# Performance work log

Measured on AMD Instinct MI355X. Metric: run time of the kernel, lower is better.

Reference implementation:

```python
import jax, jax.numpy as jnp
import numpy as np
import math
from itertools import combinations

SEQ_LEN = 8
SET_SIZE = 3
IN_DIM = 2048
OUT_DIM = 1152
WAY = 5
SHOT = 5
N_QUERIES = 200
PE_SCALE = 0.1
LN_EPS = 1e-5
NEG_INF = -1e30

TUPLES = np.array(list(combinations(range(SEQ_LEN), SET_SIZE)), dtype=np.int32)  # [56, 3]
TUPLES_LEN = TUPLES.shape[0]


def _positional_encoding(d_model, max_len):
    position = np.arange(max_len)[:, None].astype(np.float32)
    div_term = np.exp(np.arange(0, d_model, 2).astype(np.float32) * -(math.log(10000.0) / d_model))
    pe = np.zeros((max_len, d_model), dtype=np.float32)
    pe[:, 0::2] = np.sin(position * div_term) * PE_SCALE
    pe[:, 1::2] = np.cos(position * div_term) * PE_SCALE
    return jnp.asarray(pe)

PE = _positional_encoding(IN_DIM, int(SEQ_LEN * 1.5))


def setup_inputs() -> dict:
    key = jax.random.key(0)
    ks = jax.random.split(key, 6)
    support_set = jax.random.normal(ks[0], (WAY * SHOT, SEQ_LEN, IN_DIM), dtype=jnp.float32)
    queries = jax.random.normal(ks[1], (N_QUERIES, SEQ_LEN, IN_DIM), dtype=jnp.float32)
    support_labels = jnp.repeat(jnp.arange(WAY, dtype=jnp.int32), SHOT)  # [25]
    Wk = jax.random.normal(ks[2], (IN_DIM * SET_SIZE, OUT_DIM), dtype=jnp.float32) * 0.02
    bk = jnp.zeros((OUT_DIM,), dtype=jnp.float32)
    Wv = jax.random.normal(ks[3], (IN_DIM * SET_SIZE, OUT_DIM), dtype=jnp.float32) * 0.02
    bv = jnp.zeros((OUT_DIM,), dtype=jnp.float32)
    ln_g = jnp.ones((OUT_DIM,), dtype=jnp.float32)
    ln_b = jnp.zeros((OUT_DIM,), dtype=jnp.float32)
    return {"support_set": support_set, "support_labels": support_labels, "queries": queries,
            "Wk": Wk, "bk": bk, "Wv": Wv, "bv": bv, "ln_g": ln_g, "ln_b": ln_b}


def _layernorm(x, g, b):
    mu = jnp.mean(x, axis=-1, keepdims=True)
    var = jnp.var(x, axis=-1, keepdims=True)
    return (x - mu) * jax.lax.rsqrt(var + LN_EPS) * g + b


def _tuple_features(x):
    # x: [N, SEQ_LEN, IN_DIM]; add PE (dropout is identity at inference), gather frame tuples.
    n = x.shape[0]
    x = x + PE[None, :x.shape[1], :]
    return x[:, TUPLES, :].reshape(n, TUPLES_LEN, SET_SIZE * IN_DIM)  # [N, 56, 6144]


def reference(support_set, support_labels, queries, Wk, bk, Wv, bv, ln_g, ln_b):
    n_q = queries.shape[0]
    s_feat = _tuple_features(support_set)   # [S, T, 6144]
    q_feat = _tuple_features(queries)       # [Q, T, 6144]

    sk = _layernorm(s_feat @ Wk + bk, ln_g, ln_b)  # [S, T, D]
    qk = _layernorm(q_feat @ Wk + bk, ln_g, ln_b)  # [Q, T, D]
    sv = s_feat @ Wv + bv                           # [S, T, D]
    qv = q_feat @ Wv + bv                           # [Q, T, D]

    # scores between every query tuple and every support tuple
    scores = jnp.einsum('qtd,skd->qtsk', qk, sk) / math.sqrt(OUT_DIM)  # [Q, T, S, T]

    # per-class masked softmax over (support clips of class c) x (support tuples)
    class_mask = support_labels[None, :] == jnp.arange(WAY, dtype=support_labels.dtype)[:, None]  # [WAY, S]
    masked = scores[None] + jnp.where(class_mask[:, None, None, :, None], 0.0, NEG_INF)  # [WAY, Q, T, S, T]
    attn = jax.nn.softmax(masked.reshape(WAY, n_q, TUPLES_LEN, -1), axis=-1)
    attn = attn.reshape(WAY, n_q, TUPLES_LEN, -1, TUPLES_LEN)  # [WAY, Q, T, S, T]

    proto = jnp.einsum('cqtsk,skd->cqtd', attn, sv)  # [WAY, Q, T, D]
    diff = qv[None] - proto                           # [WAY, Q, T, D]
    dist = -jnp.sum(diff * diff, axis=(2, 3)) / TUPLES_LEN  # [WAY, Q]
    return dist.T  # logits [Q, WAY]
```

## Files before the change

### kernel.cpp

```cpp
#include <hip/hip_runtime.h>
#include <math.h>

#define SEQ_LEN 8
#define IN_DIM 2048
#define OUT_DIM 1152
#define NTUP 56
#define NSUP 25
#define NQ 200
#define WAY 5
#define SFRAMES 200
#define NFRAMES 1800
#define SROWS 1400
#define QROWS 11200
#define AT_STRIDE 1440
#define KC 288
#define ALD 296

typedef __attribute__((ext_vector_type(8))) short short8;
typedef __attribute__((ext_vector_type(4))) float f32x4;

__device__ __constant__ int TUP[NTUP][3] = {
{0,1,2},{0,1,3},{0,1,4},{0,1,5},{0,1,6},{0,1,7},
{0,2,3},{0,2,4},{0,2,5},{0,2,6},{0,2,7},
{0,3,4},{0,3,5},{0,3,6},{0,3,7},
{0,4,5},{0,4,6},{0,4,7},
{0,5,6},{0,5,7},
{0,6,7},
{1,2,3},{1,2,4},{1,2,5},{1,2,6},{1,2,7},
{1,3,4},{1,3,5},{1,3,6},{1,3,7},
{1,4,5},{1,4,6},{1,4,7},
{1,5,6},{1,5,7},
{1,6,7},
{2,3,4},{2,3,5},{2,3,6},{2,3,7},
{2,4,5},{2,4,6},{2,4,7},
{2,5,6},{2,5,7},
{2,6,7},
{3,4,5},{3,4,6},{3,4,7},
{3,5,6},{3,5,7},
{3,6,7},
{4,5,6},{4,5,7},
{4,6,7},
{5,6,7}};

__device__ __forceinline__ unsigned short f2bf(float x) {
  union { float f; unsigned int u; } v; v.f = x;
  unsigned int r = v.u + 0x7fffu + ((v.u >> 16) & 1u);
  return (unsigned short)(r >> 16);
}
__device__ __forceinline__ float bf2f(unsigned short s) {
  union { float f; unsigned int u; } v; v.u = ((unsigned int)s) << 16;
  return v.f;
}

__device__ __forceinline__ void gll16(const void* g, void* l) {
  __builtin_amdgcn_global_load_lds(
      (const __attribute__((address_space(1))) unsigned int*)g,
      (__attribute__((address_space(3))) unsigned int*)l, 16, 0, 0);
}

#define VMCNT(N) asm volatile("s_waitcnt vmcnt(" #N ")" ::: "memory")

__device__ __forceinline__ void pbar() {
  asm volatile("" ::: "memory");
  __builtin_amdgcn_s_barrier();
  asm volatile("" ::: "memory");
}

#define APB_OFF   0UL
#define WT_OFF    7372800UL
#define PB_OFF    35684352UL
#define QKB_OFF   60567552UL
#define SKB_OFF   86372352UL
#define QVB_OFF   89597952UL
#define SVB_OFF   115402752UL
#define G2_OFF    118628352UL
#define SCB_OFF   119457792UL
#define G1B_OFF   151713792UL
#define QNORM_OFF 183969792UL
#define RANK_OFF  184014592UL

__global__ __launch_bounds__(256) void k_pre(const float* __restrict__ S,
                                             const float* __restrict__ Q,
                                             const float* __restrict__ Wk,
                                             const float* __restrict__ Wv,
                                             const int* __restrict__ labels,
                                             unsigned short* __restrict__ APb,
                                             unsigned short* __restrict__ WT,
                                             int* __restrict__ rank,
                                             float* __restrict__ outz) {
  __shared__ float t[32][33];
  int b = blockIdx.x, tid = threadIdx.x;
  if (b < NFRAMES) {
    int frame = b;
    int e8 = tid * 8;
    int pos = frame & 7;
    const float c0 = -logf(10000.0f) / (float)IN_DIM;
    float pe[8];
#pragma unroll
    for (int p = 0; p < 4; ++p) {
      float dt = expf((float)(e8 + 2 * p) * c0);
      float arg = (float)pos * dt;
      pe[2 * p] = sinf(arg) * 0.1f;
      pe[2 * p + 1] = cosf(arg) * 0.1f;
    }
    const float* src = (frame < SFRAMES) ? (S + (size_t)frame * IN_DIM + e8)
                                         : (Q + (size_t)(frame - SFRAMES) * IN_DIM + e8);
    float4 x0 = ((const float4*)src)[0], x1 = ((const float4*)src)[1];
    short8 o;
    o[0] = (short)f2bf(x0.x + pe[0]); o[1] = (short)f2bf(x0.y + pe[1]);
    o[2] = (short)f2bf(x0.z + pe[2]); o[3] = (short)f2bf(x0.w + pe[3]);
    o[4] = (short)f2bf(x1.x + pe[4]); o[5] = (short)f2bf(x1.y + pe[5]);
    o[6] = (short)f2bf(x1.z + pe[6]); o[7] = (short)f2bf(x1.w + pe[7]);
    *(short8*)(APb + (size_t)frame * IN_DIM + e8) = o;
  } else if (b < NFRAMES + 13824) {
    int z = b - NFRAMES;
    int bz = z / (64 * 36); int rem = z % (64 * 36);
    int by = rem / 64, bx = rem % 64;
    int w = bz / 3, j = bz % 3;
    const float* W = w ? Wv : Wk;
    int k0 = bx * 32, d0 = by * 32;
    int tx = tid & 31, ty = tid >> 5;
#pragma unroll
    for (int i = 0; i < 4; ++i) {
      int k = k0 + ty + i * 8;
      t[ty + i * 8][tx] = W[(size_t)(j * IN_DIM + k) * OUT_DIM + d0 + tx];
    }
    __syncthreads();
    int colbase = w * 3456 + j * 1152 + d0;
#pragma unroll
    for (int i = 0; i < 4; ++i) {
      int d = ty + i * 8;
      WT[(size_t)(colbase + d) * IN_DIM + k0 + tx] = f2bf(t[tx][d]);
    }
  } else {
    for (int i = tid; i < NQ * WAY; i += 256) outz[i] = 0.f;
    if (tid == 0) {
      for (int s = 0; s < NSUP; ++s) {
        int r = 0;
        for (int s2 = 0; s2 < NSUP; ++s2)
          r += (labels[s2] < labels[s]) || (labels[s2] == labels[s] && s2 < s);
        rank[s] = r;
      }
    }
  }
}

__device__ __forceinline__ void mfma_core(const short* __restrict__ A, int lda, int maxA,
                                          const short* __restrict__ B, int ldb, int maxB,
                                          int K, short* lds, f32x4 (&acc)[4][4]) {
  int tid = threadIdx.x;
  int lane = tid & 63, wave = tid >> 6;
  int wm = wave & 1, wn = wave >> 1;
  int col = lane & 15, quad = lane >> 4;
  int s0 = tid, s1 = tid + 256;
  int r0 = s0 >> 2, r1 = s1 >> 2;
  int o0 = (s0 & 3) * 8, o1 = (s1 & 3) * 8;
  const short* a0p = A + (size_t)min(r0, maxA) * lda + o0;
  const short* a1p = A + (size_t)min(r1, maxA) * lda + o1;
  const short* b0p = B + (size_t)min(r0, maxB) * ldb + o0;
  const short* b1p = B + (size_t)min(r1, maxB) * ldb + o1;
  const int nt = K >> 5;

#define STAGE(t)                                     \
  do {                                               \
    short* buf_ = lds + (((t) & 3) << 13);           \
    int k0_ = (t) << 5;                              \
    gll16(a0p + k0_, buf_ + s0 * 8);                 \
    gll16(a1p + k0_, buf_ + s1 * 8);                 \
    gll16(b0p + k0_, buf_ + 4096 + s0 * 8);          \
    gll16(b1p + k0_, buf_ + 4096 + s1 * 8);          \
  } while (0)

  STAGE(0);
  STAGE(1);
  VMCNT(4);
  pbar();

  for (int t = 0; t < nt; ++t) {
    if (t + 2 < nt) STAGE(t + 2);
    const short* As = lds + ((t & 3) << 13);
    const short* Bs = As + 4096;
    short8 af[4], bf[4];
#pragma unroll
    for (int i = 0; i < 4; ++i)
      af[i] = *(const short8*)(As + (wm * 64 + i * 16 + col) * 32 + quad * 8);
#pragma unroll
    for (int j = 0; j < 4; ++j)
      bf[j] = *(const short8*)(Bs + (wn * 64 + j * 16 + col) * 32 + quad * 8);
    __builtin_amdgcn_s_setprio(1);
#pragma unroll
    for (int i = 0; i < 4; ++i)
#pragma unroll
      for (int j = 0; j < 4; ++j)
        acc[i][j] = __builtin_amdgcn_mfma_f32_16x16x32_bf16(af[i], bf[j], acc[i][j], 0, 0, 0);
    __builtin_amdgcn_s_setprio(0);
    if (t + 2 < nt) VMCNT(4);
    else            VMCNT(0);
    pbar();
  }
#undef STAGE
}

__global__ __launch_bounds__(256) void k_gemm1(const unsigned short* __restrict__ APb,
                                               const unsigned short* __restrict__ WT,
                                               unsigned short* __restrict__ Pb) {
  __shared__ short lds[32768];
  int row0 = blockIdx.y * 128, col0 = blockIdx.x * 128;
  f32x4 acc[4][4];
#pragma unroll
  for (int i = 0; i < 4; ++i)
#pragma unroll
    for (int j = 0; j < 4; ++j) acc[i][j] = (f32x4)(0.f);
  mfma_core((const short*)APb + (size_t)row0 * IN_DIM, IN_DIM, min(127, NFRAMES - 1 - row0),
            (const short*)WT + (size_t)col0 * IN_DIM, IN_DIM, 127,
            IN_DIM, lds, acc);
  int lane = threadIdx.x & 63, wave = threadIdx.x >> 6;
  int wm = wave & 1, wn = wave >> 1, col = lane & 15, quad = lane >> 4;
#pragma unroll
  for (int i = 0; i < 4; ++i)
#pragma unroll
    for (int r = 0; r < 4; ++r) {
      int gr = row0 + wm * 64 + i * 16 + quad * 4 + r;
      if (gr >= NFRAMES) continue;
#pragma unroll
      for (int j = 0; j < 4; ++j)
        Pb[(size_t)gr * 6912 + col0 + wn * 64 + j * 16 + col] = f2bf(acc[i][j][r]);
    }
}

__global__ __launch_bounds__(256) void k_combine(const unsigned short* __restrict__ Pb,
                                                 const float* __restrict__ bk,
                                                 const float* __restrict__ bv,
                                                 const float* __restrict__ g,
                                                 const float* __restrict__ bb,
                                                 const int* __restrict__ rank,
                                                 unsigned short* __restrict__ SKb,
                                                 unsigned short* __restrict__ QKb,
                                                 unsigned short* __restrict__ SVb,
                                                 unsigned short* __restrict__ QVb,
                                                 float* __restrict__ qnorm) {
  __shared__ short L[8 * 3456];
  int n = blockIdx.x, w = blockIdx.y;
  int tid = threadIdx.x;
  bool sup = n < NSUP;
  int fbase = sup ? n * SEQ_LEN : SFRAMES + (n - NSUP) * SEQ_LEN;
  for (int i = 0; i < 14; ++i) {
    int idx = tid + 256 * i;
    if (idx < 3456) {
      int fr = idx / 432, off = (idx - fr * 432) * 8;
      *(short8*)(L + fr * 3456 + off) =
          *(const short8*)(Pb + (size_t)(fbase + fr) * 6912 + w * 3456 + off);
    }
  }
  __syncthreads();
  int wave = tid >> 6, lane = tid & 63;
  const float* bias = w ? bv : bk;
  float2 bi[9], gg[9], bbv[9];
#pragma unroll
  for (int i = 0; i < 9; ++i) {
    int p = lane + 64 * i;
    bi[i] = *(const float2*)(bias + 2 * p);
    if (w == 0) {
      gg[i] = *(const float2*)(g + 2 * p);
      bbv[i] = *(const float2*)(bb + 2 * p);
    }
  }
  int obase = sup ? rank[n] * NTUP : (n - NSUP) * NTUP;
  const unsigned int* Lu = (const unsigned int*)L;
  for (int t = wave; t < NTUP; t += 4) {
    int b0 = (TUP[t][0] * 3456) >> 1;
    int b1 = (TUP[t][1] * 3456 + 1152) >> 1;
    int b2 = (TUP[t][2] * 3456 + 2304) >> 1;
    float va[18];
    float sum = 0.f, sq = 0.f;
#pragma unroll
    for (int i = 0; i < 9; ++i) {
      int p = lane + 64 * i;
      unsigned int u0 = Lu[b0 + p], u1 = Lu[b1 + p], u2 = Lu[b2 + p];
      float a = bf2f((unsigned short)u0) + bf2f((unsigned short)u1) +
                bf2f((unsigned short)u2) + bi[i].x;
      float b = bf2f((unsigned short)(u0 >> 16)) + bf2f((unsigned short)(u1 >> 16)) +
                bf2f((unsigned short)(u2 >> 16)) + bi[i].y;
      va[2 * i] = a; va[2 * i + 1] = b;
      sum += a + b;
      sq += a * a + b * b;
    }
#pragma unroll
    for (int o = 32; o; o >>= 1) {
      sum += __shfl_xor(sum, o);
      sq += __shfl_xor(sq, o);
    }
    int orow = obase + t;
    if (w == 0) {
      float mean = sum * (1.f / OUT_DIM);
      float var = sq * (1.f / OUT_DIM) - mean * mean;
      float inv = rsqrtf(var + 1e-5f);
      unsigned short* outp = (sup ? SKb : QKb) + (size_t)orow * OUT_DIM;
#pragma unroll
      for (int i = 0; i < 9; ++i) {
        int p = lane + 64 * i;
        unsigned int lo = f2bf((va[2 * i] - mean) * inv * gg[i].x + bbv[i].x);
        unsigned int hi = f2bf((va[2 * i + 1] - mean) * inv * gg[i].y + bbv[i].y);
        *(unsigned int*)(outp + 2 * p) = lo | (hi << 16);
      }
    } else {
      unsigned short* outp = (sup ? SVb : QVb) + (size_t)orow * OUT_DIM;
#pragma unroll
      for (int i = 0; i < 9; ++i) {
        int p = lane + 64 * i;
        unsigned int lo = f2bf(va[2 * i]);
        unsigned int hi = f2bf(va[2 * i + 1]);
        *(unsigned int*)(outp + 2 * p) = lo | (hi << 16);
      }
      if (!sup && lane == 0) qnorm[orow] = sq;
    }
  }
}

__global__ __launch_bounds__(256) void k_rowgemm(const unsigned short* __restrict__ QKb,
                                                 const unsigned short* __restrict__ SKb,
                                                 const unsigned short* __restrict__ QVb,
                                                 const unsigned short* __restrict__ SVb,
                                                 unsigned short* __restrict__ SCb,
                                                 unsigned short* __restrict__ G1b,
                                                 unsigned short* __restrict__ G2) {
  __shared__ short lds[32768];
  int L = blockIdx.x;
  f32x4 acc[4][4];
#pragma unroll
  for (int i = 0; i < 4; ++i)
#pragma unroll
    for (int j = 0; j < 4; ++j) acc[i][j] = (f32x4)(0.f);
  int lane = threadIdx.x & 63, wave = threadIdx.x >> 6;
  int wm = wave & 1, wn = wave >> 1, col = lane & 15, quad = lane >> 4;

  if (L < 1936) {
    int l = L, g1 = 0;
    if (l >= 968) { g1 = 1; l -= 968; }
    int rowSub = l & 7, t = l >> 3;
    int colIdx = t % 11, rowGroup = t / 11;
    int row0 = (rowGroup * 8 + rowSub) << 7;
    int col0 = colIdx << 7;
    const unsigned short* Am = g1 ? QVb : QKb;
    const unsigned short* Bm = g1 ? SVb : SKb;
    mfma_core((const short*)Am + (size_t)row0 * OUT_DIM, OUT_DIM, min(127, QROWS - 1 - row0),
              (const short*)Bm + (size_t)col0 * OUT_DIM, OUT_DIM, min(127, SROWS - 1 - col0),
              OUT_DIM, lds, acc);
    unsigned short* outp = g1 ? G1b : SCb;
    const float scl = g1 ? 1.0f : 0.029462782549439483f;
#pragma unroll
    for (int i = 0; i < 4; ++i)
#pragma unroll
      for (int r = 0; r < 4; ++r) {
        int gr = row0 + wm * 64 + i * 16 + quad * 4 + r;
        if (gr >= QROWS) continue;
#pragma unroll
        for (int j = 0; j < 4; ++j) {
          int gc = col0 + wn * 64 + j * 16 + col;
          if (gc < SROWS) {
            int c = gc / 280;
            outp[(size_t)gr * AT_STRIDE + gc + c * 8] = f2bf(acc[i][j][r] * scl);
          }
        }
      }
  } else {
    int l = L - 1936;
    int c = l / 9, rem = l % 9;
    int i0 = (rem / 3) << 7, j0 = (rem % 3) << 7;
    const short* base = (const short*)SVb + (size_t)c * 280 * OUT_DIM;
    mfma_core(base + (size_t)i0 * OUT_DIM, OUT_DIM, min(127, 279 - i0),
              base + (size_t)j0 * OUT_DIM, OUT_DIM, min(127, 279 - j0),
              OUT_DIM, lds, acc);
    unsigned short* g2c = G2 + (size_t)c * KC * KC;
#pragma unroll
    for (int i = 0; i < 4; ++i)
#pragma unroll
      for (int r = 0; r < 4; ++r) {
        int gi = i0 + wm * 64 + i * 16 + quad * 4 + r;
        if (gi >= KC) continue;
#pragma unroll
        for (int j = 0; j < 4; ++j) {
          int gj = j0 + wn * 64 + j * 16 + col;
          if (gj < KC) g2c[(size_t)gi * KC + gj] = f2bf(acc[i][j][r]);
        }
      }
  }
}

__global__ __launch_bounds__(256) void k_attn(const unsigned short* __restrict__ SCb,
                                              const unsigned short* __restrict__ G1b,
                                              const unsigned short* __restrict__ G2,
                                              const float* __restrict__ qnorm,
                                              float* __restrict__ out) {
  __shared__ short attn[64 * ALD];
  __shared__ short Bs[64 * KC];
  __shared__ float T2n[64];
  __shared__ float Sarr[64];
  __shared__ float rowsum[64];
  __shared__ float val[64];
  int r0 = blockIdx.x * 64, c = blockIdx.y;
  int tid = threadIdx.x;

  int lr = tid >> 2, h = tid & 3;
  const unsigned short* ps = SCb + (size_t)(r0 + lr) * AT_STRIDE + c * KC;
  const unsigned short* pg = G1b + (size_t)(r0 + lr) * AT_STRIDE + c * KC;
  short8 sv[9];
  float mx = -INFINITY;
#pragma unroll
  for (int i = 0; i < 9; ++i) {
    int v = h * 9 + i;
    if (v < 35) {
      sv[i] = *(const short8*)(ps + v * 8);
#pragma unroll
      for (int j = 0; j < 8; ++j) mx = fmaxf(mx, bf2f((unsigned short)sv[i][j]));
    }
  }
  mx = fmaxf(mx, __shfl_xor(mx, 1));
  mx = fmaxf(mx, __shfl_xor(mx, 2));
  float sum = 0.f, t2 = 0.f;
#pragma unroll
  for (int i = 0; i < 9; ++i) {
    int v = h * 9 + i;
    if (v < 35) {
      short8 gv8 = *(const short8*)(pg + v * 8);
      short8 e8;
#pragma unroll
      for (int j = 0; j < 8; ++j) {
        float e = __expf(bf2f((unsigned short)sv[i][j]) - mx);
        sum += e;
        t2 += e * bf2f((unsigned short)gv8[j]);
        e8[j] = (short)f2bf(e);
      }
      *(short8*)(attn + lr * ALD + v * 8) = e8;
    } else {
      *(short8*)(attn + lr * ALD + v * 8) = (short8)0;
    }
  }
  sum += __shfl_xor(sum, 1); sum += __shfl_xor(sum, 2);
  t2 += __shfl_xor(t2, 1); t2 += __shfl_xor(t2, 2);
  if (h == 0) { Sarr[lr] = sum; T2n[lr] = t2; }
  if (tid < 64) rowsum[tid] = 0.f;
  __syncthreads();

  int lane = tid & 63, wave = tid >> 6;
  int col = lane & 15, quad = lane >> 4;
  const short* G2c = (const short*)G2 + (size_t)c * KC * KC;
  float part[4][4] = {};
  for (int j0 = 0; j0 < KC; j0 += 64) {
    int ncols = min(64, KC - j0);
    int chunks = ncols * 36;
    for (int base = 0; base < chunks; base += 256) {
      int idx = base + tid;
      if (idx < chunks) {
        int n = idx / 36, kk = idx - n * 36;
        gll16(G2c + (size_t)(j0 + n) * KC + kk * 8, Bs + idx * 8);
      }
    }
    __syncthreads();
    if (wave * 16 < ncols) {
      f32x4 acc[4];
#pragma unroll
      for (int i = 0; i < 4; ++i) acc[i] = (f32x4)(0.f);
      for (int kq = 0; kq < 9; ++kq) {
        short8 bf = *(const short8*)(Bs + (wave * 16 + col) * KC + kq * 32 + quad * 8);
#pragma unroll
        for (int i = 0; i < 4; ++i) {
          short8 af = *(const short8*)(attn + (i * 16 + col) * ALD + kq * 32 + quad * 8);
          acc[i] = __builtin_amdgcn_mfma_f32_16x16x32_bf16(af, bf, acc[i], 0, 0, 0);
        }
      }
      int gcol = j0 + wave * 16 + col;
#pragma unroll
      for (int i = 0; i < 4; ++i)
#pragma unroll
        for (int r = 0; r < 4; ++r)
          part[i][r] += bf2f((unsigned short)attn[(i * 16 + quad * 4 + r) * ALD + gcol]) *
                        acc[i][r];
    }
    __syncthreads();
  }
#pragma unroll
  for (int i = 0; i < 4; ++i)
#pragma unroll
    for (int r = 0; r < 4; ++r) {
      float s = part[i][r];
      s += __shfl_xor(s, 1); s += __shfl_xor(s, 2);
      s += __shfl_xor(s, 4); s += __shfl_xor(s, 8);
      if (col == 0) atomicAdd(&rowsum[i * 16 + quad * 4 + r], s);
    }
  __syncthreads();

  if (tid < 64) {
    float S = Sarr[tid], invS = 1.f / S;
    val[tid] = qnorm[r0 + tid] - 2.f * T2n[tid] * invS + rowsum[tid] * invS * invS;
  }
  __syncthreads();
  if (tid < 3) {
    int q = r0 / NTUP + tid;
    int lo = max(q * NTUP, r0), hi = min(q * NTUP + NTUP, r0 + 64);
    if (lo < hi && q < NQ) {
      float s = 0.f;
      for (int r = lo; r < hi; ++r) s += val[r - r0];
      atomicAdd(&out[q * WAY + c], -s * (1.f / NTUP));
    }
  }
}

extern "C" void kernel_launch(void* const* d_in, const int* in_sizes, int n_in,
                              void* d_out, int out_size, void* d_ws, size_t ws_size,
                              hipStream_t stream) {
  const float* support = (const float*)d_in[0];
  const int* labels = (const int*)d_in[1];
  const float* queries = (const float*)d_in[2];
  const float* Wk = (const float*)d_in[3];
  const float* bk = (const float*)d_in[4];
  const float* Wv = (const float*)d_in[5];
  const float* bv = (const float*)d_in[6];
  const float* ln_g = (const float*)d_in[7];
  const float* ln_b = (const float*)d_in[8];
  float* out = (float*)d_out;
  char* w8 = (char*)d_ws;

  unsigned short* APb = (unsigned short*)(w8 + APB_OFF);
  unsigned short* WT = (unsigned short*)(w8 + WT_OFF);
  unsigned short* Pb = (unsigned short*)(w8 + PB_OFF);
  unsigned short* QKb = (unsigned short*)(w8 + QKB_OFF);
  unsigned short* SKb = (unsigned short*)(w8 + SKB_OFF);
  unsigned short* QVb = (unsigned short*)(w8 + QVB_OFF);
  unsigned short* SVb = (unsigned short*)(w8 + SVB_OFF);
  unsigned short* G2 = (unsigned short*)(w8 + G2_OFF);
  unsigned short* SCb = (unsigned short*)(w8 + SCB_OFF);
  unsigned short* G1b = (unsigned short*)(w8 + G1B_OFF);
  float* QNORM = (float*)(w8 + QNORM_OFF);
  int* RANK = (int*)(w8 + RANK_OFF);

  k_pre<<<dim3(NFRAMES + 13824 + 1), dim3(256), 0, stream>>>(support, queries, Wk, Wv,
                                                             labels, APb, WT, RANK, out);
  k_gemm1<<<dim3(54, 15), dim3(256), 0, stream>>>(APb, WT, Pb);
  k_combine<<<dim3(225, 2), dim3(256), 0, stream>>>(Pb, bk, bv, ln_g, ln_b, RANK,
                                                    SKb, QKb, SVb, QVb, QNORM);
  k_rowgemm<<<dim3(1981), dim3(256), 0, stream>>>(QKb, SKb, QVb, SVb, SCb, G1b, G2);
  k_attn<<<dim3(175, 5), dim3(256), 0, stream>>>(SCb, G1b, G2, QNORM, out);
}
```

Baseline: 370.3 us.

## Use 256x128 GEMM tiles with swizzled LDS, double buffering and XCD-aware block mapping

The shared MFMA GEMM core moves from 128x128 to 256x128 output tiles, so each wave computes 128x64 and every B tile loaded into LDS is reused by twice as many rows. LDS buffering drops from a 4-slot ring to 2 slots, and the k-offset is XOR-swizzled to cut bank conflicts on the fragment reads. Block indices are remapped so that neighbouring tiles land on the same XCD for L2 locality, and occupancy is pinned at 2 blocks per CU. The risks are higher register pressure from the 8x4 accumulator array, less load/compute overlap with only two buffers, and fewer blocks to spread across CUs.

```diff
diff --git a/kernel.cpp b/kernel.cpp
--- a/kernel.cpp
+++ b/kernel.cpp
@@ -145,82 +145,86 @@
   }
 }
 
-__device__ __forceinline__ void mfma_core(const short* __restrict__ A, int lda, int maxA,
-                                          const short* __restrict__ B, int ldb, int maxB,
-                                          int K, short* lds, f32x4 (&acc)[4][4]) {
+__device__ __forceinline__ void mfma_core256(const short* __restrict__ A, int lda, int maxA,
+                                             const short* __restrict__ B, int ldb, int maxB,
+                                             int K, short* lds, f32x4 (&acc)[8][4]) {
   int tid = threadIdx.x;
   int lane = tid & 63, wave = tid >> 6;
-  int wm = wave & 1, wn = wave >> 1;
+  int wm = wave >> 1, wn = wave & 1;
   int col = lane & 15, quad = lane >> 4;
-  int s0 = tid, s1 = tid + 256;
-  int r0 = s0 >> 2, r1 = s1 >> 2;
-  int o0 = (s0 & 3) * 8, o1 = (s1 & 3) * 8;
-  const short* a0p = A + (size_t)min(r0, maxA) * lda + o0;
-  const short* a1p = A + (size_t)min(r1, maxA) * lda + o1;
-  const short* b0p = B + (size_t)min(r0, maxB) * ldb + o0;
-  const short* b1p = B + (size_t)min(r1, maxB) * ldb + o1;
+  int kq8 = (quad ^ ((col >> 1) & 3)) * 8;
+
+  int rt_ = tid >> 2;
+  int qo = ((tid & 3) ^ ((tid >> 3) & 3)) * 8;
+  const short* a0p = A + (size_t)min(rt_,       maxA) * lda + qo;
+  const short* a1p = A + (size_t)min(rt_ + 64,  maxA) * lda + qo;
+  const short* a2p = A + (size_t)min(rt_ + 128, maxA) * lda + qo;
+  const short* a3p = A + (size_t)min(rt_ + 192, maxA) * lda + qo;
+  const short* b0p = B + (size_t)min(rt_,       maxB) * ldb + qo;
+  const short* b1p = B + (size_t)min(rt_ + 64,  maxB) * ldb + qo;
   const int nt = K >> 5;
 
 #define STAGE(t)                                     \
   do {                                               \
-    short* buf_ = lds + (((t) & 3) << 13);           \
+    short* buf_ = lds + (((t) & 1) * 12288);         \
     int k0_ = (t) << 5;                              \
-    gll16(a0p + k0_, buf_ + s0 * 8);                 \
-    gll16(a1p + k0_, buf_ + s1 * 8);                 \
-    gll16(b0p + k0_, buf_ + 4096 + s0 * 8);          \
-    gll16(b1p + k0_, buf_ + 4096 + s1 * 8);          \
+    gll16(a0p + k0_, buf_ + (size_t)tid * 8);        \
+    gll16(a1p + k0_, buf_ + (size_t)(tid + 256) * 8);\
+    gll16(a2p + k0_, buf_ + (size_t)(tid + 512) * 8);\
+    gll16(a3p + k0_, buf_ + (size_t)(tid + 768) * 8);\
+    gll16(b0p + k0_, buf_ + 8192 + (size_t)tid * 8); \
+    gll16(b1p + k0_, buf_ + 8192 + (size_t)(tid + 256) * 8);\
   } while (0)
 
   STAGE(0);
-  STAGE(1);
-  VMCNT(4);
-  pbar();
-
   for (int t = 0; t < nt; ++t) {
-    if (t + 2 < nt) STAGE(t + 2);
-    const short* As = lds + ((t & 3) << 13);
-    const short* Bs = As + 4096;
-    short8 af[4], bf[4];
-#pragma unroll
-    for (int i = 0; i < 4; ++i)
-      af[i] = *(const short8*)(As + (wm * 64 + i * 16 + col) * 32 + quad * 8);
+    if (t + 1 < nt) { STAGE(t + 1); VMCNT(6); }
+    else            { VMCNT(0); }
+    pbar();
+    const short* As = lds + ((t & 1) * 12288);
+    const short* Bs = As + 8192;
+    short8 af[8], bf[4];
+#pragma unroll
+    for (int i = 0; i < 8; ++i)
+      af[i] = *(const short8*)(As + (wm * 128 + i * 16 + col) * 32 + kq8);
 #pragma unroll
     for (int j = 0; j < 4; ++j)
-      bf[j] = *(const short8*)(Bs + (wn * 64 + j * 16 + col) * 32 + quad * 8);
+      bf[j] = *(const short8*)(Bs + (wn * 64 + j * 16 + col) * 32 + kq8);
     __builtin_amdgcn_s_setprio(1);
 #pragma unroll
-    for (int i = 0; i < 4; ++i)
+    for (int i = 0; i < 8; ++i)
 #pragma unroll
       for (int j = 0; j < 4; ++j)
         acc[i][j] = __builtin_amdgcn_mfma_f32_16x16x32_bf16(af[i], bf[j], acc[i][j], 0, 0, 0);
     __builtin_amdgcn_s_setprio(0);
-    if (t + 2 < nt) VMCNT(4);
-    else            VMCNT(0);
     pbar();
   }
 #undef STAGE
 }
 
-__global__ __launch_bounds__(256) void k_gemm1(const unsigned short* __restrict__ APb,
-                                               const unsigned short* __restrict__ WT,
-                                               unsigned short* __restrict__ Pb) {
-  __shared__ short lds[32768];
-  int row0 = blockIdx.y * 128, col0 = blockIdx.x * 128;
-  f32x4 acc[4][4];
-#pragma unroll
-  for (int i = 0; i < 4; ++i)
+__global__ __launch_bounds__(256, 2) void k_gemm1(const unsigned short* __restrict__ APb,
+                                                  const unsigned short* __restrict__ WT,
+                                                  unsigned short* __restrict__ Pb) {
+  __shared__ short lds[24576];
+  int o = blockIdx.x;
+  int L = (o & 7) * 54 + (o >> 3);
+  int rt = L / 54, ct = L % 54;
+  int row0 = rt << 8, col0 = ct << 7;
+  f32x4 acc[8][4];
+#pragma unroll
+  for (int i = 0; i < 8; ++i)
 #pragma unroll
     for (int j = 0; j < 4; ++j) acc[i][j] = (f32x4)(0.f);
-  mfma_core((const short*)APb + (size_t)row0 * IN_DIM, IN_DIM, min(127, NFRAMES - 1 - row0),
-            (const short*)WT + (size_t)col0 * IN_DIM, IN_DIM, 127,
-            IN_DIM, lds, acc);
+  mfma_core256((const short*)APb + (size_t)row0 * IN_DIM, IN_DIM, min(255, NFRAMES - 1 - row0),
+               (const short*)WT + (size_t)col0 * IN_DIM, IN_DIM, 127,
+               IN_DIM, lds, acc);
   int lane = threadIdx.x & 63, wave = threadIdx.x >> 6;
-  int wm = wave & 1, wn = wave >> 1, col = lane & 15, quad = lane >> 4;
-#pragma unroll
-  for (int i = 0; i < 4; ++i)
+  int wm = wave >> 1, wn = wave & 1, col = lane & 15, quad = lane >> 4;
+#pragma unroll
+  for (int i = 0; i < 8; ++i)
 #pragma unroll
     for (int r = 0; r < 4; ++r) {
-      int gr = row0 + wm * 64 + i * 16 + quad * 4 + r;
+      int gr = row0 + wm * 128 + i * 16 + quad * 4 + r;
       if (gr >= NFRAMES) continue;
 #pragma unroll
       for (int j = 0; j < 4; ++j)
@@ -317,42 +321,41 @@
   }
 }
 
-__global__ __launch_bounds__(256) void k_rowgemm(const unsigned short* __restrict__ QKb,
-                                                 const unsigned short* __restrict__ SKb,
-                                                 const unsigned short* __restrict__ QVb,
-                                                 const unsigned short* __restrict__ SVb,
-                                                 unsigned short* __restrict__ SCb,
-                                                 unsigned short* __restrict__ G1b,
-                                                 unsigned short* __restrict__ G2) {
-  __shared__ short lds[32768];
-  int L = blockIdx.x;
-  f32x4 acc[4][4];
-#pragma unroll
-  for (int i = 0; i < 4; ++i)
+__global__ __launch_bounds__(256, 2) void k_rowgemm(const unsigned short* __restrict__ QKb,
+                                                    const unsigned short* __restrict__ SKb,
+                                                    const unsigned short* __restrict__ QVb,
+                                                    const unsigned short* __restrict__ SVb,
+                                                    unsigned short* __restrict__ SCb,
+                                                    unsigned short* __restrict__ G1b,
+                                                    unsigned short* __restrict__ G2) {
+  __shared__ short lds[24576];
+  int o = blockIdx.x;
+  int xcd = o & 7, idx = o >> 3;
+  int L = (xcd < 6 ? xcd * 125 : 750 + (xcd - 6) * 124) + idx;
+  f32x4 acc[8][4];
+#pragma unroll
+  for (int i = 0; i < 8; ++i)
 #pragma unroll
     for (int j = 0; j < 4; ++j) acc[i][j] = (f32x4)(0.f);
   int lane = threadIdx.x & 63, wave = threadIdx.x >> 6;
-  int wm = wave & 1, wn = wave >> 1, col = lane & 15, quad = lane >> 4;
-
-  if (L < 1936) {
-    int l = L, g1 = 0;
-    if (l >= 968) { g1 = 1; l -= 968; }
-    int rowSub = l & 7, t = l >> 3;
-    int colIdx = t % 11, rowGroup = t / 11;
-    int row0 = (rowGroup * 8 + rowSub) << 7;
-    int col0 = colIdx << 7;
+  int wm = wave >> 1, wn = wave & 1, col = lane & 15, quad = lane >> 4;
+
+  if (L < 968) {
+    int g1 = L >= 484; int l = g1 ? L - 484 : L;
+    int rt = l / 11, ct = l % 11;
+    int row0 = rt << 8, col0 = ct << 7;
     const unsigned short* Am = g1 ? QVb : QKb;
     const unsigned short* Bm = g1 ? SVb : SKb;
-    mfma_core((const short*)Am + (size_t)row0 * OUT_DIM, OUT_DIM, min(127, QROWS - 1 - row0),
-              (const short*)Bm + (size_t)col0 * OUT_DIM, OUT_DIM, min(127, SROWS - 1 - col0),
-              OUT_DIM, lds, acc);
+    mfma_core256((const short*)Am + (size_t)row0 * OUT_DIM, OUT_DIM, min(255, QROWS - 1 - row0),
+                 (const short*)Bm + (size_t)col0 * OUT_DIM, OUT_DIM, min(127, SROWS - 1 - col0),
+                 OUT_DIM, lds, acc);
     unsigned short* outp = g1 ? G1b : SCb;
     const float scl = g1 ? 1.0f : 0.029462782549439483f;
 #pragma unroll
-    for (int i = 0; i < 4; ++i)
+    for (int i = 0; i < 8; ++i)
 #pragma unroll
       for (int r = 0; r < 4; ++r) {
-        int gr = row0 + wm * 64 + i * 16 + quad * 4 + r;
+        int gr = row0 + wm * 128 + i * 16 + quad * 4 + r;
         if (gr >= QROWS) continue;
 #pragma unroll
         for (int j = 0; j < 4; ++j) {
@@ -364,19 +367,20 @@
         }
       }
   } else {
-    int l = L - 1936;
-    int c = l / 9, rem = l % 9;
-    int i0 = (rem / 3) << 7, j0 = (rem % 3) << 7;
+    int l = L - 968;
+    int c = l / 6, rem = l % 6;
+    int rt = rem / 3, ct = rem % 3;
+    int i0 = rt << 8, j0 = ct << 7;
     const short* base = (const short*)SVb + (size_t)c * 280 * OUT_DIM;
-    mfma_core(base + (size_t)i0 * OUT_DIM, OUT_DIM, min(127, 279 - i0),
-              base + (size_t)j0 * OUT_DIM, OUT_DIM, min(127, 279 - j0),
-              OUT_DIM, lds, acc);
+    mfma_core256(base + (size_t)i0 * OUT_DIM, OUT_DIM, 279 - i0,
+                 base + (size_t)j0 * OUT_DIM, OUT_DIM, min(127, 279 - j0),
+                 OUT_DIM, lds, acc);
     unsigned short* g2c = G2 + (size_t)c * KC * KC;
 #pragma unroll
-    for (int i = 0; i < 4; ++i)
+    for (int i = 0; i < 8; ++i)
 #pragma unroll
       for (int r = 0; r < 4; ++r) {
-        int gi = i0 + wm * 64 + i * 16 + quad * 4 + r;
+        int gi = i0 + wm * 128 + i * 16 + quad * 4 + r;
         if (gi >= KC) continue;
 #pragma unroll
         for (int j = 0; j < 4; ++j) {
@@ -536,9 +540,9 @@
 
   k_pre<<<dim3(NFRAMES + 13824 + 1), dim3(256), 0, stream>>>(support, queries, Wk, Wv,
                                                              labels, APb, WT, RANK, out);
-  k_gemm1<<<dim3(54, 15), dim3(256), 0, stream>>>(APb, WT, Pb);
+  k_gemm1<<<dim3(432), dim3(256), 0, stream>>>(APb, WT, Pb);
   k_combine<<<dim3(225, 2), dim3(256), 0, stream>>>(Pb, bk, bv, ln_g, ln_b, RANK,
                                                     SKb, QKb, SVb, QVb, QNORM);
-  k_rowgemm<<<dim3(1981), dim3(256), 0, stream>>>(QKb, SKb, QVb, SVb, SCb, G1b, G2);
+  k_rowgemm<<<dim3(998), dim3(256), 0, stream>>>(QKb, SKb, QVb, SVb, SCb, G1b, G2);
   k_attn<<<dim3(175, 5), dim3(256), 0, stream>>>(SCb, G1b, G2, QNORM, out);
 }
```

Result: faster. 348.5 us (-5.9%).
